# Kernel tuning notes

Hardware: AMD Instinct MI355X
Metric: run time of the kernel (lower is better)

The kernel has to match this reference:

```python
import jax, jax.numpy as jnp
import numpy as np

N = 30000      # nodes
E = 480000     # edges (before self-loops)
D = 100        # hidden_dim / in_channels
H = 4          # heads
PH = 100       # per-head dim
L = 6          # layers
G = 128        # graphs in batch
NUM_ATOM = 100
OUT_DIM = 64


def _xavier(k, shape, gain=1.0):
    fan_in, fan_out = shape[-1], shape[-2]
    lim = gain * np.sqrt(6.0 / (fan_in + fan_out))
    return jax.random.uniform(k, shape, jnp.float32, -lim, lim)


def setup_inputs() -> dict:
    key = jax.random.key(0)
    ks = jax.random.split(key, 12)
    x = jax.random.randint(ks[0], (N,), 0, NUM_ATOM)
    edge_index = jax.random.randint(ks[1], (2, E), 0, N)
    edge_attr = jax.random.normal(ks[2], (E, D), dtype=jnp.float32)
    batch = jnp.sort(jax.random.randint(ks[3], (N,), 0, G))
    emb = _xavier(ks[4], (NUM_ATOM, D))
    W = _xavier(ks[5], (L, H * PH, D))
    We = _xavier(ks[6], (L, H * PH, D))
    a = _xavier(ks[7], (L, H, 2 * PH), gain=1.414)
    ln_g = jnp.ones((L, D), jnp.float32)
    ln_b = jnp.zeros((L, D), jnp.float32)
    w1 = _xavier(ks[8], (OUT_DIM, D))
    b1 = jnp.zeros((OUT_DIM,), jnp.float32)
    w2 = _xavier(ks[9], (1, OUT_DIM))
    b2 = jnp.zeros((1,), jnp.float32)
    return dict(x=x, edge_index=edge_index, edge_attr=edge_attr, batch=batch,
                emb=emb, W=W, We=We, a=a, ln_g=ln_g, ln_b=ln_b,
                w1=w1, b1=b1, w2=w2, b2=b2)


def _forward(x, edge_index, edge_attr, batch, emb, W, We, a, ln_g, ln_b, w1, b1, w2, b2):
    n = x.shape[0]
    loop = jnp.arange(n)
    src = jnp.concatenate([edge_index[0], loop])            # [E']
    dst = jnp.concatenate([edge_index[1], loop])            # [E']  (target, softmax key)
    ea = jnp.concatenate([edge_attr, jnp.zeros((n, D), edge_attr.dtype)], axis=0)  # self-loop attr = 0
    h = emb[x]                                              # [N, D]
    for l in range(L):
        hx = (h @ W[l].T).reshape(n, H, PH)                 # [N, H, PH]
        he = (ea @ We[l].T).reshape(-1, H, PH)              # [E', H, PH]
        a_i, a_j = a[l][:, :PH], a[l][:, PH:]               # [H, PH] each
        # alpha = sum(a * [x_i ; x_j + edge_attr]) split into two dots
        score_i = jnp.einsum('nhd,hd->nh', hx, a_i)         # [N, H]
        xj = hx[src]                                        # [E', H, PH]
        alpha = score_i[dst] + jnp.einsum('ehd,hd->eh', xj + he, a_j)  # [E', H]
        alpha = jnp.where(alpha > 0, alpha, 0.2 * alpha)    # leaky_relu(0.2)
        # segment softmax over edges grouped by target node (every node has a self-loop)
        amax = jax.ops.segment_max(alpha, dst, num_segments=n)
        alpha = jnp.exp(alpha - amax[dst])
        denom = jax.ops.segment_sum(alpha, dst, num_segments=n)
        alpha = alpha / (denom[dst] + 1e-16)
        msg = (xj * alpha[..., None]).sum(axis=1)           # [E', PH] (heads summed, per module)
        aggr = jax.ops.segment_sum(msg, dst, num_segments=n)  # [N, PH]
        # LayerNorm(D), eps=1e-5
        mu = aggr.mean(-1, keepdims=True)
        var = ((aggr - mu) ** 2).mean(-1, keepdims=True)
        y = (aggr - mu) / jnp.sqrt(var + 1e-5) * ln_g[l] + ln_b[l]
        y = jax.nn.elu(y)                                   # dropout = identity (eval)
        h = y + h
    # global mean pool over graphs
    s = jax.ops.segment_sum(h, batch, num_segments=G)
    cnt = jax.ops.segment_sum(jnp.ones((n, 1), h.dtype), batch, num_segments=G)
    pooled = s / jnp.maximum(cnt, 1.0)
    hh = pooled @ w1.T + b1                                 # [G, 64]
    out = hh @ w2.T + b2                                    # [G, 1]
    return out, hh


def reference(x, edge_index, edge_attr, batch, emb, W, We, a, ln_g, ln_b, w1, b1, w2, b2):
    return _forward(x, edge_index, edge_attr, batch, emb, W, We, a, ln_g, ln_b, w1, b1, w2, b2)
```

## Files before the change

kernel.cpp:

```cpp
#include <hip/hip_runtime.h>
#include <cstdint>
#include <cstddef>

#define N_NODES 30000
#define N_EDGES 480000
#define EP_EDGES (N_EDGES + N_NODES)
#define DIM 100
#define NH 4
#define NL 6
#define NG 128
#define KP 416

#define OFF_H       0u
#define OFF_AGG2    12000000u
#define OFF_EID     12000000u
#define OFF_DEG     14040000u
#define OFF_CURS    14160000u
#define OFF_POOL    12000000u
#define OFF_CNT     12051200u
#define OFF_SCI     60000000u
#define OFF_SCJ     60480000u
#define OFF_ESC     60960000u
#define OFF_CWIJ    85440000u
#define OFF_CWE     85459200u
#define OFF_WR      85469184u
#define OFF_INDPTR  86429184u
#define OFF_CSRS    86549248u
#define OFF_BSUM    88589248u

typedef _Float16 half8 __attribute__((ext_vector_type(8)));
typedef float f32x4 __attribute__((ext_vector_type(4)));

static __device__ __forceinline__ unsigned short f2h(float f) {
  return __builtin_bit_cast(unsigned short, (_Float16)f);
}
static __device__ __forceinline__ float h2f(unsigned short u) {
  return (float)__builtin_bit_cast(_Float16, u);
}

__global__ __launch_bounds__(256) void k_init(const int* __restrict__ x,
                                              const float* __restrict__ emb,
                                              float* __restrict__ h,
                                              int* __restrict__ deg, int* __restrict__ cursor) {
  int tid = blockIdx.x * 256 + threadIdx.x;
  if (tid < N_NODES * DIM) {
    int n = tid / DIM;
    int d = tid - n * DIM;
    h[tid] = emb[x[n] * DIM + d];
  }
  if (tid < N_NODES) { deg[tid] = 0; cursor[tid] = 0; }
}

__global__ __launch_bounds__(256) void k_fold(const float* __restrict__ W,
                                              const float* __restrict__ We,
                                              const float* __restrict__ a,
                                              float* __restrict__ cWij, float* __restrict__ cWe2) {
  int tid = blockIdx.x * 256 + threadIdx.x;
  if (tid < NL * DIM * 8) {
    int l = tid / 800, r = tid % 800;
    int k = r >> 3, c = r & 7;
    int hh = c & 3, isJ = c >> 2;
    const float* wp = W + (size_t)(l * 400 + hh * 100) * 100 + k;
    const float* ap = a + (size_t)(l * 4 + hh) * 200 + isJ * 100;
    float s = 0.f;
    for (int d = 0; d < 100; ++d) s += wp[(size_t)d * 100] * ap[d];
    cWij[l * 800 + k * 8 + c] = s;
  } else if (tid < NL * DIM * 8 + DIM * 24) {
    int m = tid - NL * DIM * 8;
    int k = m / 24, c = m % 24;
    int l = c >> 2, hh = c & 3;
    const float* wp = We + (size_t)(l * 400 + hh * 100) * 100 + k;
    const float* ap = a + (size_t)(l * 4 + hh) * 200 + 100;
    float s = 0.f;
    for (int d = 0; d < 100; ++d) s += wp[(size_t)d * 100] * ap[d];
    cWe2[((k >> 2) * 24 + c) * 4 + (k & 3)] = s;
  }
}

__global__ __launch_bounds__(256) void k_bfrag(const float* __restrict__ W,
                                               unsigned short* __restrict__ Bfrag) {
  int tid = blockIdx.x * 256 + threadIdx.x;
  if (tid >= NL * 7 * 13 * 64 * 8) return;
  int j = tid & 7;
  int lane = (tid >> 3) & 63;
  int rest = tid >> 9;
  int ks = rest % 13;
  int rest2 = rest / 13;
  int ct = rest2 % 7;
  int l = rest2 / 7;
  int k = ks * 32 + ((lane >> 4) << 3) + j;
  int n = ct * 16 + (lane & 15);
  float v = 0.f;
  if (k < 400 && n < 100) {
    int hh = k / 100, kk = k - hh * 100;
    v = W[(size_t)(l * 400 + hh * 100 + n) * 100 + kk];
  }
  Bfrag[tid] = f2h(v);
}

__global__ __launch_bounds__(256) void k_deg(const int* __restrict__ ei, int* __restrict__ deg) {
  int tid = blockIdx.x * 256 + threadIdx.x;
  if (tid >= EP_EDGES) return;
  int dstn = (tid < N_EDGES) ? ei[N_EDGES + tid] : (tid - N_EDGES);
  atomicAdd(&deg[dstn], 1);
}

__global__ __launch_bounds__(1024) void k_scan1(const int* __restrict__ deg,
                                                int* __restrict__ indptr, int* __restrict__ bsum) {
  __shared__ int s[1024];
  int t = threadIdx.x;
  int i = blockIdx.x * 1024 + t;
  int v = (i < N_NODES) ? deg[i] : 0;
  s[t] = v;
  __syncthreads();
  for (int off = 1; off < 1024; off <<= 1) {
    int tmp = (t >= off) ? s[t - off] : 0;
    __syncthreads();
    s[t] += tmp;
    __syncthreads();
  }
  if (i < N_NODES) indptr[i + 1] = s[t];
  if (t == 1023) bsum[blockIdx.x] = s[1023];
}
__global__ __launch_bounds__(64) void k_scan2(int* __restrict__ bsum) {
  int t = threadIdx.x;
  int v = (t < 30) ? bsum[t] : 0;
  int inc = v;
  for (int off = 1; off < 64; off <<= 1) {
    int up = __shfl_up(inc, off);
    if (t >= off) inc += up;
  }
  if (t < 30) bsum[t] = inc - v;
}
__global__ __launch_bounds__(1024) void k_scan3(int* __restrict__ indptr,
                                                const int* __restrict__ bsum) {
  int i = blockIdx.x * 1024 + threadIdx.x;
  if (i < N_NODES) indptr[i + 1] += bsum[blockIdx.x];
  if (i == 0) indptr[0] = 0;
}

__global__ __launch_bounds__(256) void k_scatter(const int* __restrict__ ei,
                                                 const int* __restrict__ indptr,
                                                 int* __restrict__ cursor,
                                                 int* __restrict__ csr_src,
                                                 int* __restrict__ csr_eid) {
  int tid = blockIdx.x * 256 + threadIdx.x;
  if (tid >= EP_EDGES) return;
  int dstn = (tid < N_EDGES) ? ei[N_EDGES + tid] : (tid - N_EDGES);
  int srcn = (tid < N_EDGES) ? ei[tid] : (tid - N_EDGES);
  int p = indptr[dstn] + atomicAdd(&cursor[dstn], 1);
  csr_src[p] = srcn;
  csr_eid[p] = (tid < N_EDGES) ? tid : -1;
}

__global__ __launch_bounds__(256) void k_escore(const float* __restrict__ ea,
                                                const float* __restrict__ cWe2,
                                                const int* __restrict__ csr_eid,
                                                unsigned short* __restrict__ esc) {
  int slot = blockIdx.x * 256 + threadIdx.x;
  int e = (slot < EP_EDGES) ? csr_eid[slot] : -1;
  float acc[24];
#pragma unroll
  for (int c = 0; c < 24; ++c) acc[c] = 0.f;
  if (e >= 0) {
    const float4* rp = (const float4*)(ea + (size_t)e * DIM);
    for (int k4 = 0; k4 < 25; ++k4) {
      float4 x = rp[k4];
      const float4* wp = (const float4*)(cWe2 + k4 * 96);
#pragma unroll
      for (int c = 0; c < 24; ++c) {
        float4 w = wp[c];
        acc[c] = fmaf(x.w, w.w, fmaf(x.z, w.z, fmaf(x.y, w.y, fmaf(x.x, w.x, acc[c]))));
      }
    }
  }
  if (slot < EP_EDGES) {
#pragma unroll
    for (int l = 0; l < NL; ++l) {
      ushort4 o;
      o.x = f2h(acc[l * 4 + 0]); o.y = f2h(acc[l * 4 + 1]);
      o.z = f2h(acc[l * 4 + 2]); o.w = f2h(acc[l * 4 + 3]);
      *(ushort4*)(esc + ((size_t)l * EP_EDGES + slot) * 4) = o;
    }
  }
}

__global__ __launch_bounds__(256) void k_score(const float* __restrict__ h,
                                               const float* __restrict__ cw,
                                               float* __restrict__ sc_i, float* __restrict__ sc_j) {
  __shared__ __align__(16) float s[DIM * 8];
  for (int i = threadIdx.x; i < DIM * 8; i += 256) s[i] = cw[i];
  __syncthreads();
  int n = blockIdx.x * 256 + threadIdx.x;
  if (n >= N_NODES) return;
  float acc[8] = {0.f, 0.f, 0.f, 0.f, 0.f, 0.f, 0.f, 0.f};
  const float* hr = h + (size_t)n * DIM;
  for (int k4 = 0; k4 < 25; ++k4) {
    float4 v = *(const float4*)(hr + k4 * 4);
    float vv[4] = {v.x, v.y, v.z, v.w};
#pragma unroll
    for (int kk = 0; kk < 4; ++kk) {
      const float* sr = s + (k4 * 4 + kk) * 8;
#pragma unroll
      for (int c = 0; c < 8; ++c) acc[c] += vv[kk] * sr[c];
    }
  }
  *(float4*)(sc_i + (size_t)n * 4) = make_float4(acc[0], acc[1], acc[2], acc[3]);
  *(float4*)(sc_j + (size_t)n * 4) = make_float4(acc[4], acc[5], acc[6], acc[7]);
}

#define ALPHA_P(pp)                                                                  \
  int s_ = csr_src[pp];                                                              \
  float4 sj_ = *(const float4*)(sc_j + (size_t)s_ * 4);                              \
  ushort4 eb_ = *(const ushort4*)(esc_l + (size_t)(pp) * 4);                         \
  float a0 = si.x + sj_.x + h2f(eb_.x); a0 = a0 > 0.f ? a0 : 0.2f * a0;              \
  float a1 = si.y + sj_.y + h2f(eb_.y); a1 = a1 > 0.f ? a1 : 0.2f * a1;              \
  float a2 = si.z + sj_.z + h2f(eb_.z); a2 = a2 > 0.f ? a2 : 0.2f * a2;              \
  float a3 = si.w + sj_.w + h2f(eb_.w); a3 = a3 > 0.f ? a3 : 0.2f * a3;

__global__ __launch_bounds__(256) void k_aggr(const float* __restrict__ h,
                                              const float* __restrict__ sc_i,
                                              const float* __restrict__ sc_j,
                                              const unsigned short* __restrict__ esc_l,
                                              const int* __restrict__ indptr,
                                              const int* __restrict__ csr_src,
                                              unsigned short* __restrict__ agg2h) {
  __shared__ __align__(16) uint4 s_pack[4][64];
  int wave = threadIdx.x >> 6;
  int lane = threadIdx.x & 63;
  int n = blockIdx.x * 4 + wave;
  int start = indptr[n], end = indptr[n + 1];
  int deg = end - start;
  float4 si = *(const float4*)(sc_i + (size_t)n * 4);
  float A0 = 0.f, A1 = 0.f, A2 = 0.f, A3 = 0.f;
  float B0 = 0.f, B1 = 0.f, B2 = 0.f, B3 = 0.f;
  bool has2 = lane < (DIM - 64);

  if (deg <= 64) {
    int p = start + lane;
    bool act = p < end;
    int srcr = 0;
    float a0 = -1e30f, a1 = -1e30f, a2 = -1e30f, a3 = -1e30f;
    if (act) {
      int s2 = csr_src[p];
      float4 sj2 = *(const float4*)(sc_j + (size_t)s2 * 4);
      ushort4 eb2 = *(const ushort4*)(esc_l + (size_t)p * 4);
      a0 = si.x + sj2.x + h2f(eb2.x); a0 = a0 > 0.f ? a0 : 0.2f * a0;
      a1 = si.y + sj2.y + h2f(eb2.y); a1 = a1 > 0.f ? a1 : 0.2f * a1;
      a2 = si.z + sj2.z + h2f(eb2.z); a2 = a2 > 0.f ? a2 : 0.2f * a2;
      a3 = si.w + sj2.w + h2f(eb2.w); a3 = a3 > 0.f ? a3 : 0.2f * a3;
      srcr = s2;
    }
    float m0 = a0, m1 = a1, m2 = a2, m3 = a3;
    for (int off = 32; off; off >>= 1) {
      m0 = fmaxf(m0, __shfl_xor(m0, off));
      m1 = fmaxf(m1, __shfl_xor(m1, off));
      m2 = fmaxf(m2, __shfl_xor(m2, off));
      m3 = fmaxf(m3, __shfl_xor(m3, off));
    }
    float e0 = act ? __expf(a0 - m0) : 0.f;
    float e1 = act ? __expf(a1 - m1) : 0.f;
    float e2 = act ? __expf(a2 - m2) : 0.f;
    float e3 = act ? __expf(a3 - m3) : 0.f;
    float d0 = e0, d1 = e1, d2 = e2, d3 = e3;
    for (int off = 32; off; off >>= 1) {
      d0 += __shfl_xor(d0, off); d1 += __shfl_xor(d1, off);
      d2 += __shfl_xor(d2, off); d3 += __shfl_xor(d3, off);
    }
    float w0 = e0 * (1.f / (d0 + 1e-16f));
    float w1 = e1 * (1.f / (d1 + 1e-16f));
    float w2 = e2 * (1.f / (d2 + 1e-16f));
    float w3 = e3 * (1.f / (d3 + 1e-16f));
    uint4 pk;
    pk.x = (unsigned)srcr;
    pk.y = (unsigned)f2h(w0) | ((unsigned)f2h(w1) << 16);
    pk.z = (unsigned)f2h(w2) | ((unsigned)f2h(w3) << 16);
    pk.w = 0u;
    s_pack[wave][lane] = pk;
    for (int j = 0; j < deg; ++j) {
      uint4 pk2 = s_pack[wave][j];
      int sj2 = (int)pk2.x;
      float q0 = h2f((unsigned short)(pk2.y & 0xffffu));
      float q1 = h2f((unsigned short)(pk2.y >> 16));
      float q2 = h2f((unsigned short)(pk2.z & 0xffffu));
      float q3 = h2f((unsigned short)(pk2.z >> 16));
      const float* hr = h + (size_t)sj2 * DIM;
      float hv0 = hr[lane];
      float hv1 = has2 ? hr[64 + lane] : 0.f;
      A0 += q0 * hv0; A1 += q1 * hv0; A2 += q2 * hv0; A3 += q3 * hv0;
      B0 += q0 * hv1; B1 += q1 * hv1; B2 += q2 * hv1; B3 += q3 * hv1;
    }
  } else {
    float m0 = -1e30f, m1 = -1e30f, m2 = -1e30f, m3 = -1e30f;
    for (int p = start + lane; p < end; p += 64) {
      ALPHA_P(p)
      (void)s_;
      m0 = fmaxf(m0, a0); m1 = fmaxf(m1, a1); m2 = fmaxf(m2, a2); m3 = fmaxf(m3, a3);
    }
    for (int off = 32; off; off >>= 1) {
      m0 = fmaxf(m0, __shfl_xor(m0, off));
      m1 = fmaxf(m1, __shfl_xor(m1, off));
      m2 = fmaxf(m2, __shfl_xor(m2, off));
      m3 = fmaxf(m3, __shfl_xor(m3, off));
    }
    float d0 = 0.f, d1 = 0.f, d2 = 0.f, d3 = 0.f;
    for (int p = start + lane; p < end; p += 64) {
      ALPHA_P(p)
      (void)s_;
      d0 += __expf(a0 - m0); d1 += __expf(a1 - m1);
      d2 += __expf(a2 - m2); d3 += __expf(a3 - m3);
    }
    for (int off = 32; off; off >>= 1) {
      d0 += __shfl_xor(d0, off); d1 += __shfl_xor(d1, off);
      d2 += __shfl_xor(d2, off); d3 += __shfl_xor(d3, off);
    }
    float i0 = 1.f / (d0 + 1e-16f), i1 = 1.f / (d1 + 1e-16f);
    float i2 = 1.f / (d2 + 1e-16f), i3 = 1.f / (d3 + 1e-16f);
    for (int base = start; base < end; base += 64) {
      int cntv = min(64, end - base);
      int p = base + lane;
      float w0 = 0.f, w1 = 0.f, w2 = 0.f, w3 = 0.f;
      int srcr = 0;
      if (p < end) {
        ALPHA_P(p)
        w0 = __expf(a0 - m0) * i0; w1 = __expf(a1 - m1) * i1;
        w2 = __expf(a2 - m2) * i2; w3 = __expf(a3 - m3) * i3;
        srcr = s_;
      }
      for (int j = 0; j < cntv; ++j) {
        int sj2 = __shfl(srcr, j);
        float q0 = __shfl(w0, j), q1 = __shfl(w1, j);
        float q2 = __shfl(w2, j), q3 = __shfl(w3, j);
        const float* hr = h + (size_t)sj2 * DIM;
        float hv0 = hr[lane];
        float hv1 = has2 ? hr[64 + lane] : 0.f;
        A0 += q0 * hv0; A1 += q1 * hv0; A2 += q2 * hv0; A3 += q3 * hv0;
        B0 += q0 * hv1; B1 += q1 * hv1; B2 += q2 * hv1; B3 += q3 * hv1;
      }
    }
  }
  unsigned short* outp = agg2h + (size_t)n * KP;
  outp[lane] = f2h(A0); outp[100 + lane] = f2h(A1);
  outp[200 + lane] = f2h(A2); outp[300 + lane] = f2h(A3);
  if (has2) {
    outp[64 + lane] = f2h(B0); outp[164 + lane] = f2h(B1);
    outp[264 + lane] = f2h(B2); outp[364 + lane] = f2h(B3);
  }
  if (lane < KP - 400) outp[400 + lane] = 0;
}

__global__ __launch_bounds__(256) void k_gemm2(const _Float16* __restrict__ agg2h,
                                               const _Float16* __restrict__ Bfrag_l,
                                               const float* __restrict__ lg,
                                               const float* __restrict__ lb,
                                               float* __restrict__ h) {
  int t = threadIdx.x;
  int lane = t & 63;
  int w = t >> 6;
  int c = lane & 15;
  int quad = lane >> 4;
  int nb = blockIdx.x * 64 + w * 16;

  f32x4 acc[7];
#pragma unroll
  for (int ct = 0; ct < 7; ++ct) acc[ct] = (f32x4){0.f, 0.f, 0.f, 0.f};

  const _Float16* arow = agg2h + (size_t)(nb + c) * KP + quad * 8;
#pragma unroll
  for (int ks = 0; ks < 13; ++ks) {
    half8 a = *(const half8*)(arow + ks * 32);
    const _Float16* bp = Bfrag_l + (size_t)(ks * 64 + lane) * 8;
#pragma unroll
    for (int ct = 0; ct < 7; ++ct) {
      half8 b = *(const half8*)(bp + (size_t)ct * 13 * 64 * 8);
      acc[ct] = __builtin_amdgcn_mfma_f32_16x16x32_f16(a, b, acc[ct], 0, 0, 0);
    }
  }

  float gv[7], bv[7];
#pragma unroll
  for (int ct = 0; ct < 7; ++ct) {
    int col = ct * 16 + c;
    gv[ct] = (col < DIM) ? lg[col] : 0.f;
    bv[ct] = (col < DIM) ? lb[col] : 0.f;
  }
  bool c4 = c < 4;
#pragma unroll
  for (int r = 0; r < 4; ++r) {
    int n = nb + quad * 4 + r;
    float v[7];
#pragma unroll
    for (int ct = 0; ct < 7; ++ct) v[ct] = acc[ct][r];
    float s = v[0] + v[1] + v[2] + v[3] + v[4] + v[5] + (c4 ? v[6] : 0.f);
    s += __shfl_xor(s, 1); s += __shfl_xor(s, 2);
    s += __shfl_xor(s, 4); s += __shfl_xor(s, 8);
    float mu = s * 0.01f;
    float dv[7];
    float s2 = 0.f;
#pragma unroll
    for (int ct = 0; ct < 6; ++ct) { dv[ct] = v[ct] - mu; s2 += dv[ct] * dv[ct]; }
    dv[6] = c4 ? (v[6] - mu) : 0.f;
    s2 += dv[6] * dv[6];
    s2 += __shfl_xor(s2, 1); s2 += __shfl_xor(s2, 2);
    s2 += __shfl_xor(s2, 4); s2 += __shfl_xor(s2, 8);
    float rstd = rsqrtf(s2 * 0.01f + 1e-5f);
    if (n < N_NODES) {
      float* hp = h + (size_t)n * DIM;
#pragma unroll
      for (int ct = 0; ct < 7; ++ct) {
        int col = ct * 16 + c;
        if (ct < 6 || c4) {
          float y = dv[ct] * rstd * gv[ct] + bv[ct];
          y = y > 0.f ? y : (__expf(y) - 1.f);
          hp[col] += y;
        }
      }
    }
  }
}

__global__ __launch_bounds__(128) void k_pool(const float* __restrict__ h,
                                              const int* __restrict__ batch,
                                              float* __restrict__ pooled, float* __restrict__ cnt) {
  int d = threadIdx.x;
  int n0 = blockIdx.x * 64;
  int n1 = min(n0 + 64, N_NODES);
  if (n0 >= N_NODES) return;
  int curg = -1;
  float acc = 0.f, c = 0.f;
  for (int n = n0; n < n1; ++n) {
    int g = batch[n];
    if (g != curg) {
      if (curg >= 0) {
        if (d < 100) atomicAdd(&pooled[(size_t)curg * DIM + d], acc);
        if (d == 0) atomicAdd(&cnt[curg], c);
      }
      curg = g; acc = 0.f; c = 0.f;
    }
    if (d < 100) acc += h[(size_t)n * DIM + d];
    c += 1.f;
  }
  if (curg >= 0) {
    if (d < 100) atomicAdd(&pooled[(size_t)curg * DIM + d], acc);
    if (d == 0) atomicAdd(&cnt[curg], c);
  }
}

__global__ __launch_bounds__(64) void k_mlp(const float* __restrict__ pooled,
                                            const float* __restrict__ cnt,
                                            const float* __restrict__ w1, const float* __restrict__ b1,
                                            const float* __restrict__ w2, const float* __restrict__ b2,
                                            float* __restrict__ out) {
  int g = blockIdx.x;
  int j = threadIdx.x;
  float invc = 1.0f / fmaxf(cnt[g], 1.0f);
  const float* pr = pooled + (size_t)g * DIM;
  const float* wr = w1 + (size_t)j * DIM;
  float acc = 0.f;
  for (int k = 0; k < DIM; ++k) acc += pr[k] * wr[k];
  float hh = acc * invc + b1[j];
  out[NG + g * 64 + j] = hh;
  float v = hh * w2[j];
  for (int off = 32; off; off >>= 1) v += __shfl_xor(v, off);
  if (j == 0) out[g] = v + b2[0];
}

extern "C" void kernel_launch(void* const* d_in, const int* in_sizes, int n_in,
                              void* d_out, int out_size, void* d_ws, size_t ws_size,
                              hipStream_t stream) {
  (void)in_sizes; (void)n_in; (void)out_size; (void)ws_size;
  const int* x = (const int*)d_in[0];
  const int* ei = (const int*)d_in[1];
  const float* ea = (const float*)d_in[2];
  const int* batch = (const int*)d_in[3];
  const float* emb = (const float*)d_in[4];
  const float* W = (const float*)d_in[5];
  const float* We = (const float*)d_in[6];
  const float* a = (const float*)d_in[7];
  const float* ln_g = (const float*)d_in[8];
  const float* ln_b = (const float*)d_in[9];
  const float* w1 = (const float*)d_in[10];
  const float* b1 = (const float*)d_in[11];
  const float* w2 = (const float*)d_in[12];
  const float* b2 = (const float*)d_in[13];
  float* outp = (float*)d_out;

  char* ws = (char*)d_ws;
  float* h = (float*)(ws + OFF_H);
  unsigned short* agg2h = (unsigned short*)(ws + OFF_AGG2);
  int* csr_eid = (int*)(ws + OFF_EID);
  int* deg = (int*)(ws + OFF_DEG);
  int* cursor = (int*)(ws + OFF_CURS);
  float* pooled = (float*)(ws + OFF_POOL);
  float* cnt = (float*)(ws + OFF_CNT);
  float* sc_i = (float*)(ws + OFF_SCI);
  float* sc_j = (float*)(ws + OFF_SCJ);
  unsigned short* esc = (unsigned short*)(ws + OFF_ESC);
  float* cWij = (float*)(ws + OFF_CWIJ);
  float* cWe2 = (float*)(ws + OFF_CWE);
  unsigned short* Bfrag = (unsigned short*)(ws + OFF_WR);
  int* indptr = (int*)(ws + OFF_INDPTR);
  int* csr_src = (int*)(ws + OFF_CSRS);
  int* bsum = (int*)(ws + OFF_BSUM);

  k_init<<<11719, 256, 0, stream>>>(x, emb, h, deg, cursor);
  k_fold<<<29, 256, 0, stream>>>(W, We, a, cWij, cWe2);
  k_bfrag<<<1092, 256, 0, stream>>>(W, Bfrag);
  k_deg<<<1993, 256, 0, stream>>>(ei, deg);
  k_scan1<<<30, 1024, 0, stream>>>(deg, indptr, bsum);
  k_scan2<<<1, 64, 0, stream>>>(bsum);
  k_scan3<<<30, 1024, 0, stream>>>(indptr, bsum);
  k_scatter<<<1993, 256, 0, stream>>>(ei, indptr, cursor, csr_src, csr_eid);
  k_escore<<<1993, 256, 0, stream>>>(ea, cWe2, csr_eid, esc);

  for (int l = 0; l < NL; ++l) {
    k_score<<<118, 256, 0, stream>>>(h, cWij + l * 800, sc_i, sc_j);
    k_aggr<<<7500, 256, 0, stream>>>(h, sc_i, sc_j, esc + (size_t)l * EP_EDGES * 4,
                                     indptr, csr_src, agg2h);
    k_gemm2<<<469, 256, 0, stream>>>((const _Float16*)agg2h,
                                     (const _Float16*)(Bfrag + (size_t)l * 7 * 13 * 64 * 8),
                                     ln_g + l * 100, ln_b + l * 100, h);
  }

  hipMemsetAsync(ws + OFF_POOL, 0, 51200 + 512, stream);
  k_pool<<<469, 128, 0, stream>>>(h, batch, pooled, cnt);
  k_mlp<<<128, 64, 0, stream>>>(pooled, cnt, w1, b1, w2, b2, outp);
}
```

Measured before the change: 955.9 us.

## Stream edge attributes in original order via async LDS loads, then permute scores

```diff
diff --git a/kernel.cpp b/kernel.cpp
--- a/kernel.cpp
+++ b/kernel.cpp
@@ -16,6 +16,7 @@
 #define OFF_EID     12000000u
 #define OFF_DEG     14040000u
 #define OFF_CURS    14160000u
+#define OFF_ETMP    16000000u
 #define OFF_POOL    12000000u
 #define OFF_CNT     12051200u
 #define OFF_SCI     60000000u
@@ -31,6 +32,9 @@
 typedef _Float16 half8 __attribute__((ext_vector_type(8)));
 typedef float f32x4 __attribute__((ext_vector_type(4)));
 
+typedef __attribute__((address_space(1))) const float gl_cfloat;
+typedef __attribute__((address_space(3))) float lds_float;
+
 static __device__ __forceinline__ unsigned short f2h(float f) {
   return __builtin_bit_cast(unsigned short, (_Float16)f);
 }
@@ -54,7 +58,7 @@
 __global__ __launch_bounds__(256) void k_fold(const float* __restrict__ W,
                                               const float* __restrict__ We,
                                               const float* __restrict__ a,
-                                              float* __restrict__ cWij, float* __restrict__ cWe2) {
+                                              float* __restrict__ cWij, float* __restrict__ cWe) {
   int tid = blockIdx.x * 256 + threadIdx.x;
   if (tid < NL * DIM * 8) {
     int l = tid / 800, r = tid % 800;
@@ -73,7 +77,7 @@
     const float* ap = a + (size_t)(l * 4 + hh) * 200 + 100;
     float s = 0.f;
     for (int d = 0; d < 100; ++d) s += wp[(size_t)d * 100] * ap[d];
-    cWe2[((k >> 2) * 24 + c) * 4 + (k & 3)] = s;
+    cWe[c * 104 + k] = s;
   }
 }
 
@@ -153,36 +157,89 @@
   csr_eid[p] = (tid < N_EDGES) ? tid : -1;
 }
 
-__global__ __launch_bounds__(256) void k_escore(const float* __restrict__ ea,
-                                                const float* __restrict__ cWe2,
-                                                const int* __restrict__ csr_eid,
-                                                unsigned short* __restrict__ esc) {
-  int slot = blockIdx.x * 256 + threadIdx.x;
-  int e = (slot < EP_EDGES) ? csr_eid[slot] : -1;
-  float acc[24];
-#pragma unroll
-  for (int c = 0; c < 24; ++c) acc[c] = 0.f;
+__global__ __launch_bounds__(384) void k_escore(const float* __restrict__ ea,
+                                                const float* __restrict__ cWe,
+                                                unsigned short* __restrict__ esc_tmp) {
+  __shared__ __align__(16) float s_ea[2][6400];
+  int t = threadIdx.x;
+  int slot = t & 63;
+  int lg = __builtin_amdgcn_readfirstlane(t >> 6);
+  const float* wl = cWe + (lg * 4) * 104;
+
+  int tile = blockIdx.x;
+  {
+    const float* src = ea + (size_t)tile * 6400;
+#pragma unroll
+    for (int it = 0; it < 4; ++it) {
+      int e4 = it * 384 + t;
+      __builtin_amdgcn_global_load_lds((gl_cfloat*)(src + e4 * 4),
+                                       (lds_float*)(&s_ea[0][e4 * 4]), 16, 0, 0);
+    }
+    if (t < 64) {
+      int e4 = 1536 + t;
+      __builtin_amdgcn_global_load_lds((gl_cfloat*)(src + e4 * 4),
+                                       (lds_float*)(&s_ea[0][e4 * 4]), 16, 0, 0);
+    }
+  }
+  __syncthreads();
+
+  int buf = 0;
+  for (; tile < N_EDGES / 64; tile += gridDim.x) {
+    int nxt = tile + (int)gridDim.x;
+    if (nxt < N_EDGES / 64) {
+      const float* src = ea + (size_t)nxt * 6400;
+#pragma unroll
+      for (int it = 0; it < 4; ++it) {
+        int e4 = it * 384 + t;
+        __builtin_amdgcn_global_load_lds((gl_cfloat*)(src + e4 * 4),
+                                         (lds_float*)(&s_ea[buf ^ 1][e4 * 4]), 16, 0, 0);
+      }
+      if (t < 64) {
+        int e4 = 1536 + t;
+        __builtin_amdgcn_global_load_lds((gl_cfloat*)(src + e4 * 4),
+                                         (lds_float*)(&s_ea[buf ^ 1][e4 * 4]), 16, 0, 0);
+      }
+    }
+    const float* r0 = &s_ea[buf][slot * 100];
+    float acc0 = 0.f, acc1 = 0.f, acc2 = 0.f, acc3 = 0.f;
+#pragma unroll
+    for (int k4 = 0; k4 < 25; ++k4) {
+      float4 x = *(const float4*)(r0 + k4 * 4);
+      float4 w0 = *(const float4*)(wl + 0 * 104 + k4 * 4);
+      float4 w1 = *(const float4*)(wl + 1 * 104 + k4 * 4);
+      float4 w2 = *(const float4*)(wl + 2 * 104 + k4 * 4);
+      float4 w3 = *(const float4*)(wl + 3 * 104 + k4 * 4);
+      acc0 = fmaf(x.w, w0.w, fmaf(x.z, w0.z, fmaf(x.y, w0.y, fmaf(x.x, w0.x, acc0))));
+      acc1 = fmaf(x.w, w1.w, fmaf(x.z, w1.z, fmaf(x.y, w1.y, fmaf(x.x, w1.x, acc1))));
+      acc2 = fmaf(x.w, w2.w, fmaf(x.z, w2.z, fmaf(x.y, w2.y, fmaf(x.x, w2.x, acc2))));
+      acc3 = fmaf(x.w, w3.w, fmaf(x.z, w3.z, fmaf(x.y, w3.y, fmaf(x.x, w3.x, acc3))));
+    }
+    ushort4 o;
+    o.x = f2h(acc0); o.y = f2h(acc1); o.z = f2h(acc2); o.w = f2h(acc3);
+    *(ushort4*)(esc_tmp + ((size_t)tile * 64 + slot) * 24 + lg * 4) = o;
+    __syncthreads();
+    buf ^= 1;
+  }
+}
+
+__global__ __launch_bounds__(256) void k_permute(const unsigned short* __restrict__ esc_tmp,
+                                                 const int* __restrict__ csr_eid,
+                                                 unsigned short* __restrict__ esc) {
+  int p = blockIdx.x * 256 + threadIdx.x;
+  if (p >= EP_EDGES) return;
+  int e = csr_eid[p];
+  ushort4 v[NL];
   if (e >= 0) {
-    const float4* rp = (const float4*)(ea + (size_t)e * DIM);
-    for (int k4 = 0; k4 < 25; ++k4) {
-      float4 x = rp[k4];
-      const float4* wp = (const float4*)(cWe2 + k4 * 96);
-#pragma unroll
-      for (int c = 0; c < 24; ++c) {
-        float4 w = wp[c];
-        acc[c] = fmaf(x.w, w.w, fmaf(x.z, w.z, fmaf(x.y, w.y, fmaf(x.x, w.x, acc[c]))));
-      }
-    }
-  }
-  if (slot < EP_EDGES) {
-#pragma unroll
-    for (int l = 0; l < NL; ++l) {
-      ushort4 o;
-      o.x = f2h(acc[l * 4 + 0]); o.y = f2h(acc[l * 4 + 1]);
-      o.z = f2h(acc[l * 4 + 2]); o.w = f2h(acc[l * 4 + 3]);
-      *(ushort4*)(esc + ((size_t)l * EP_EDGES + slot) * 4) = o;
-    }
-  }
+    const unsigned short* rp = esc_tmp + (size_t)e * 24;
+#pragma unroll
+    for (int l = 0; l < NL; ++l) v[l] = *(const ushort4*)(rp + l * 4);
+  } else {
+#pragma unroll
+    for (int l = 0; l < NL; ++l) { v[l].x = 0; v[l].y = 0; v[l].z = 0; v[l].w = 0; }
+  }
+#pragma unroll
+  for (int l = 0; l < NL; ++l)
+    *(ushort4*)(esc + ((size_t)l * EP_EDGES + p) * 4) = v[l];
 }
 
 __global__ __launch_bounds__(256) void k_score(const float* __restrict__ h,
@@ -491,27 +548,29 @@
   int* csr_eid = (int*)(ws + OFF_EID);
   int* deg = (int*)(ws + OFF_DEG);
   int* cursor = (int*)(ws + OFF_CURS);
+  unsigned short* esc_tmp = (unsigned short*)(ws + OFF_ETMP);
   float* pooled = (float*)(ws + OFF_POOL);
   float* cnt = (float*)(ws + OFF_CNT);
   float* sc_i = (float*)(ws + OFF_SCI);
   float* sc_j = (float*)(ws + OFF_SCJ);
   unsigned short* esc = (unsigned short*)(ws + OFF_ESC);
   float* cWij = (float*)(ws + OFF_CWIJ);
-  float* cWe2 = (float*)(ws + OFF_CWE);
+  float* cWe = (float*)(ws + OFF_CWE);
   unsigned short* Bfrag = (unsigned short*)(ws + OFF_WR);
   int* indptr = (int*)(ws + OFF_INDPTR);
   int* csr_src = (int*)(ws + OFF_CSRS);
   int* bsum = (int*)(ws + OFF_BSUM);
 
   k_init<<<11719, 256, 0, stream>>>(x, emb, h, deg, cursor);
-  k_fold<<<29, 256, 0, stream>>>(W, We, a, cWij, cWe2);
+  k_fold<<<29, 256, 0, stream>>>(W, We, a, cWij, cWe);
   k_bfrag<<<1092, 256, 0, stream>>>(W, Bfrag);
   k_deg<<<1993, 256, 0, stream>>>(ei, deg);
   k_scan1<<<30, 1024, 0, stream>>>(deg, indptr, bsum);
   k_scan2<<<1, 64, 0, stream>>>(bsum);
   k_scan3<<<30, 1024, 0, stream>>>(indptr, bsum);
   k_scatter<<<1993, 256, 0, stream>>>(ei, indptr, cursor, csr_src, csr_eid);
-  k_escore<<<1993, 256, 0, stream>>>(ea, cWe2, csr_eid, esc);
+  k_escore<<<1250, 384, 0, stream>>>(ea, cWe, esc_tmp);
+  k_permute<<<1993, 256, 0, stream>>>(esc_tmp, csr_eid, esc);
 
   for (int l = 0; l < NL; ++l) {
     k_score<<<118, 256, 0, stream>>>(h, cWij + l * 800, sc_i, sc_j);
```

New measurement: 864.0 us. 1.11x faster.

## Compute edge attention scores with split-fp16 MFMA in edge order, then permute

Applied to the files above, without the earlier changes.

```diff
diff --git a/kernel.cpp b/kernel.cpp
--- a/kernel.cpp
+++ b/kernel.cpp
@@ -16,19 +16,21 @@
 #define OFF_EID     12000000u
 #define OFF_DEG     14040000u
 #define OFF_CURS    14160000u
+#define OFF_ETMP    16000000u
 #define OFF_POOL    12000000u
 #define OFF_CNT     12051200u
 #define OFF_SCI     60000000u
 #define OFF_SCJ     60480000u
 #define OFF_ESC     60960000u
 #define OFF_CWIJ    85440000u
-#define OFF_CWE     85459200u
 #define OFF_WR      85469184u
 #define OFF_INDPTR  86429184u
 #define OFF_CSRS    86549248u
 #define OFF_BSUM    88589248u
+#define OFF_BW      88589376u
 
 typedef _Float16 half8 __attribute__((ext_vector_type(8)));
+typedef __fp16 fp16x2 __attribute__((ext_vector_type(2)));
 typedef float f32x4 __attribute__((ext_vector_type(4)));
 
 static __device__ __forceinline__ unsigned short f2h(float f) {
@@ -54,7 +56,8 @@
 __global__ __launch_bounds__(256) void k_fold(const float* __restrict__ W,
                                               const float* __restrict__ We,
                                               const float* __restrict__ a,
-                                              float* __restrict__ cWij, float* __restrict__ cWe2) {
+                                              float* __restrict__ cWij,
+                                              unsigned short* __restrict__ Bw) {
   int tid = blockIdx.x * 256 + threadIdx.x;
   if (tid < NL * DIM * 8) {
     int l = tid / 800, r = tid % 800;
@@ -73,7 +76,24 @@
     const float* ap = a + (size_t)(l * 4 + hh) * 200 + 100;
     float s = 0.f;
     for (int d = 0; d < 100; ++d) s += wp[(size_t)d * 100] * ap[d];
-    cWe2[((k >> 2) * 24 + c) * 4 + (k & 3)] = s;
+    _Float16 vh = (_Float16)s;
+    _Float16 vl = (_Float16)(s - (float)vh);
+    int ct = c >> 4;
+    int lane = (((k & 31) >> 3) << 4) | (c & 15);
+    int ks = k >> 5;
+    int j = k & 7;
+    Bw[(size_t)(((0 * 2 + ct) * 4 + ks) * 64 + lane) * 8 + j] = __builtin_bit_cast(unsigned short, vh);
+    Bw[(size_t)(((1 * 2 + ct) * 4 + ks) * 64 + lane) * 8 + j] = __builtin_bit_cast(unsigned short, vl);
+  } else if (tid < NL * DIM * 8 + DIM * 24 + 8192) {
+    int E = tid - (NL * DIM * 8 + DIM * 24);
+    int j = E & 7;
+    int lane = (E >> 3) & 63;
+    int rest = E >> 9;
+    int ks = rest & 3;
+    int ct = (rest >> 2) & 1;
+    int c = ct * 16 + (lane & 15);
+    int k = ks * 32 + ((lane >> 4) << 3) + j;
+    if (!(c < 24 && k < 100)) Bw[E] = 0;
   }
 }
 
@@ -153,36 +173,103 @@
   csr_eid[p] = (tid < N_EDGES) ? tid : -1;
 }
 
-__global__ __launch_bounds__(256) void k_escore(const float* __restrict__ ea,
-                                                const float* __restrict__ cWe2,
-                                                const int* __restrict__ csr_eid,
-                                                unsigned short* __restrict__ esc) {
-  int slot = blockIdx.x * 256 + threadIdx.x;
-  int e = (slot < EP_EDGES) ? csr_eid[slot] : -1;
-  float acc[24];
-#pragma unroll
-  for (int c = 0; c < 24; ++c) acc[c] = 0.f;
+__global__ __launch_bounds__(256, 4) void k_escore(const float* __restrict__ ea,
+                                                   const unsigned short* __restrict__ Bw,
+                                                   unsigned short* __restrict__ esc_tmp) {
+  __shared__ __align__(16) float s_ea[64 * 128];
+  int t = threadIdx.x;
+  int lane = t & 63;
+  int wv = t >> 6;
+
+  const half8* bp = (const half8*)Bw;
+  half8 Bh[2][4], Bl[2][4];
+#pragma unroll
+  for (int ct = 0; ct < 2; ++ct)
+#pragma unroll
+    for (int ks = 0; ks < 4; ++ks) {
+      Bh[ct][ks] = bp[((0 * 2 + ct) * 4 + ks) * 64 + lane];
+      Bl[ct][ks] = bp[((1 * 2 + ct) * 4 + ks) * 64 + lane];
+    }
+
+  int e0 = blockIdx.x * 64;
+  const float4* g4 = (const float4*)(ea + (size_t)e0 * 100);
+  for (int z = t; z < 448; z += 256) {
+    int zr = z / 7, zc = z - zr * 7;
+    int o = 400 + zc * 16;
+    *(float4*)((char*)s_ea + zr * 512 + (o ^ ((zr & 7) << 4))) = (float4){0.f, 0.f, 0.f, 0.f};
+  }
+#pragma unroll
+  for (int i = 0; i < 7; ++i) {
+    int v = i * 256 + t;
+    if (i < 6 || v < 1600) {
+      float4 val = g4[v];
+      int r = v / 25, kk = v - r * 25;
+      *(float4*)((char*)s_ea + r * 512 + ((kk * 16) ^ ((r & 7) << 4))) = val;
+    }
+  }
+  __syncthreads();
+
+  int c = lane & 15;
+  int quad = lane >> 4;
+  int lrow = wv * 16 + c;
+  int swz = (lrow & 7) << 4;
+  const char* base = (const char*)s_ea + lrow * 512;
+  f32x4 acc0 = (f32x4){0.f, 0.f, 0.f, 0.f};
+  f32x4 acc1 = (f32x4){0.f, 0.f, 0.f, 0.f};
+#pragma unroll
+  for (int ks = 0; ks < 4; ++ks) {
+    int o = ks * 128 + quad * 32;
+    float4 xa = *(const float4*)(base + ((o) ^ swz));
+    float4 xb = *(const float4*)(base + ((o + 16) ^ swz));
+    fp16x2 h0 = __builtin_amdgcn_cvt_pkrtz(xa.x, xa.y);
+    fp16x2 h1 = __builtin_amdgcn_cvt_pkrtz(xa.z, xa.w);
+    fp16x2 h2 = __builtin_amdgcn_cvt_pkrtz(xb.x, xb.y);
+    fp16x2 h3 = __builtin_amdgcn_cvt_pkrtz(xb.z, xb.w);
+    fp16x2 l0 = __builtin_amdgcn_cvt_pkrtz(xa.x - (float)h0[0], xa.y - (float)h0[1]);
+    fp16x2 l1 = __builtin_amdgcn_cvt_pkrtz(xa.z - (float)h1[0], xa.w - (float)h1[1]);
+    fp16x2 l2 = __builtin_amdgcn_cvt_pkrtz(xb.x - (float)h2[0], xb.y - (float)h2[1]);
+    fp16x2 l3 = __builtin_amdgcn_cvt_pkrtz(xb.z - (float)h3[0], xb.w - (float)h3[1]);
+    uint4 uh = {__builtin_bit_cast(unsigned, h0), __builtin_bit_cast(unsigned, h1),
+                __builtin_bit_cast(unsigned, h2), __builtin_bit_cast(unsigned, h3)};
+    uint4 ul = {__builtin_bit_cast(unsigned, l0), __builtin_bit_cast(unsigned, l1),
+                __builtin_bit_cast(unsigned, l2), __builtin_bit_cast(unsigned, l3)};
+    half8 xh = __builtin_bit_cast(half8, uh);
+    half8 xl = __builtin_bit_cast(half8, ul);
+    acc0 = __builtin_amdgcn_mfma_f32_16x16x32_f16(xh, Bh[0][ks], acc0, 0, 0, 0);
+    acc0 = __builtin_amdgcn_mfma_f32_16x16x32_f16(xl, Bh[0][ks], acc0, 0, 0, 0);
+    acc0 = __builtin_amdgcn_mfma_f32_16x16x32_f16(xh, Bl[0][ks], acc0, 0, 0, 0);
+    acc1 = __builtin_amdgcn_mfma_f32_16x16x32_f16(xh, Bh[1][ks], acc1, 0, 0, 0);
+    acc1 = __builtin_amdgcn_mfma_f32_16x16x32_f16(xl, Bh[1][ks], acc1, 0, 0, 0);
+    acc1 = __builtin_amdgcn_mfma_f32_16x16x32_f16(xh, Bl[1][ks], acc1, 0, 0, 0);
+  }
+
+  unsigned short* orow = esc_tmp + (size_t)(e0 + wv * 16 + quad * 4) * 24;
+#pragma unroll
+  for (int r = 0; r < 4; ++r) {
+    unsigned short* op = orow + r * 24;
+    op[c] = f2h(acc0[r]);
+    if (c < 8) op[16 + c] = f2h(acc1[r]);
+  }
+}
+
+__global__ __launch_bounds__(256) void k_permute(const unsigned short* __restrict__ esc_tmp,
+                                                 const int* __restrict__ csr_eid,
+                                                 unsigned short* __restrict__ esc) {
+  int p = blockIdx.x * 256 + threadIdx.x;
+  if (p >= EP_EDGES) return;
+  int e = csr_eid[p];
+  ushort4 v[NL];
   if (e >= 0) {
-    const float4* rp = (const float4*)(ea + (size_t)e * DIM);
-    for (int k4 = 0; k4 < 25; ++k4) {
-      float4 x = rp[k4];
-      const float4* wp = (const float4*)(cWe2 + k4 * 96);
-#pragma unroll
-      for (int c = 0; c < 24; ++c) {
-        float4 w = wp[c];
-        acc[c] = fmaf(x.w, w.w, fmaf(x.z, w.z, fmaf(x.y, w.y, fmaf(x.x, w.x, acc[c]))));
-      }
-    }
-  }
-  if (slot < EP_EDGES) {
-#pragma unroll
-    for (int l = 0; l < NL; ++l) {
-      ushort4 o;
-      o.x = f2h(acc[l * 4 + 0]); o.y = f2h(acc[l * 4 + 1]);
-      o.z = f2h(acc[l * 4 + 2]); o.w = f2h(acc[l * 4 + 3]);
-      *(ushort4*)(esc + ((size_t)l * EP_EDGES + slot) * 4) = o;
-    }
-  }
+    const unsigned short* rp = esc_tmp + (size_t)e * 24;
+#pragma unroll
+    for (int l = 0; l < NL; ++l) v[l] = *(const ushort4*)(rp + l * 4);
+  } else {
+#pragma unroll
+    for (int l = 0; l < NL; ++l) { v[l].x = 0; v[l].y = 0; v[l].z = 0; v[l].w = 0; }
+  }
+#pragma unroll
+  for (int l = 0; l < NL; ++l)
+    *(ushort4*)(esc + ((size_t)l * EP_EDGES + p) * 4) = v[l];
 }
 
 __global__ __launch_bounds__(256) void k_score(const float* __restrict__ h,
@@ -491,27 +578,29 @@
   int* csr_eid = (int*)(ws + OFF_EID);
   int* deg = (int*)(ws + OFF_DEG);
   int* cursor = (int*)(ws + OFF_CURS);
+  unsigned short* esc_tmp = (unsigned short*)(ws + OFF_ETMP);
   float* pooled = (float*)(ws + OFF_POOL);
   float* cnt = (float*)(ws + OFF_CNT);
   float* sc_i = (float*)(ws + OFF_SCI);
   float* sc_j = (float*)(ws + OFF_SCJ);
   unsigned short* esc = (unsigned short*)(ws + OFF_ESC);
   float* cWij = (float*)(ws + OFF_CWIJ);
-  float* cWe2 = (float*)(ws + OFF_CWE);
+  unsigned short* Bw = (unsigned short*)(ws + OFF_BW);
   unsigned short* Bfrag = (unsigned short*)(ws + OFF_WR);
   int* indptr = (int*)(ws + OFF_INDPTR);
   int* csr_src = (int*)(ws + OFF_CSRS);
   int* bsum = (int*)(ws + OFF_BSUM);
 
   k_init<<<11719, 256, 0, stream>>>(x, emb, h, deg, cursor);
-  k_fold<<<29, 256, 0, stream>>>(W, We, a, cWij, cWe2);
+  k_fold<<<61, 256, 0, stream>>>(W, We, a, cWij, Bw);
   k_bfrag<<<1092, 256, 0, stream>>>(W, Bfrag);
   k_deg<<<1993, 256, 0, stream>>>(ei, deg);
   k_scan1<<<30, 1024, 0, stream>>>(deg, indptr, bsum);
   k_scan2<<<1, 64, 0, stream>>>(bsum);
   k_scan3<<<30, 1024, 0, stream>>>(indptr, bsum);
   k_scatter<<<1993, 256, 0, stream>>>(ei, indptr, cursor, csr_src, csr_eid);
-  k_escore<<<1993, 256, 0, stream>>>(ea, cWe2, csr_eid, esc);
+  k_escore<<<7500, 256, 0, stream>>>(ea, Bw, esc_tmp);
+  k_permute<<<1993, 256, 0, stream>>>(esc_tmp, csr_eid, esc);
 
   for (int l = 0; l < NL; ++l) {
     k_score<<<118, 256, 0, stream>>>(h, cWij + l * 800, sc_i, sc_j);
```

After: 829.0 us. -13.3%, faster.
